# Optimization experiments

Measured on AMD Instinct MI355X. Metric: run time of the kernel, lower is better.

## Reference

```python
import jax, jax.numpy as jnp
import numpy as np
import math

D_MODEL = 1024
NUM_HEADS = 16
SEQ = 2048
BATCH = 2


def setup_inputs() -> dict:
    key = jax.random.key(0)
    ks = jax.random.split(key, 12)
    s = 1.0 / math.sqrt(D_MODEL)
    inp = {
        "query": jax.random.normal(ks[0], (SEQ, BATCH, D_MODEL), jnp.float32),
        "key": jax.random.normal(ks[1], (SEQ, BATCH, D_MODEL), jnp.float32),
        "value": jax.random.normal(ks[2], (SEQ, BATCH, D_MODEL), jnp.float32),
        "Wq": jax.random.normal(ks[3], (D_MODEL, D_MODEL), jnp.float32) * s,
        "bq": jax.random.normal(ks[4], (D_MODEL,), jnp.float32) * 0.01,
        "Wk": jax.random.normal(ks[5], (D_MODEL, D_MODEL), jnp.float32) * s,
        "bk": jax.random.normal(ks[6], (D_MODEL,), jnp.float32) * 0.01,
        "Wv": jax.random.normal(ks[7], (D_MODEL, D_MODEL), jnp.float32) * s,
        "bv": jax.random.normal(ks[8], (D_MODEL,), jnp.float32) * 0.01,
        "Wo": jax.random.normal(ks[9], (D_MODEL, D_MODEL), jnp.float32) * s,
        "bo": jax.random.normal(ks[10], (D_MODEL,), jnp.float32) * 0.01,
    }
    # causal (subsequent) mask: True above the diagonal means masked
    inp["attn_mask"] = jnp.triu(jnp.ones((SEQ, SEQ), bool), k=1)
    # key_padding_mask: True = padding; random lengths in [SEQ//2, SEQ]
    lengths = jax.random.randint(ks[11], (BATCH,), SEQ // 2, SEQ + 1)
    inp["key_padding_mask"] = jnp.arange(SEQ)[None, :] >= lengths[:, None]
    return inp


def reference(query, key, value, Wq, bq, Wk, bk, Wv, bv, Wo, bo, attn_mask, key_padding_mask):
    S, B, D = query.shape
    H = NUM_HEADS
    dk = D // H

    def proj_split(x, W, b):
        y = x @ W.T + b                      # [S, B, D]
        return y.reshape(S, B, H, dk).transpose(1, 2, 0, 3)  # [B, H, S, dk]

    q = proj_split(query, Wq, bq)
    k = proj_split(key, Wk, bk)
    v = proj_split(value, Wv, bv)

    scores = jnp.einsum("bhqd,bhkd->bhqk", q, k) / jnp.sqrt(jnp.float32(dk))
    mask = key_padding_mask[:, None, None, :] | attn_mask[None, None, :, :]
    scores = jnp.where(mask, -jnp.inf, scores)
    p = jax.nn.softmax(scores, axis=-1)       # [B, H, S, S]
    x = jnp.einsum("bhqk,bhkd->bhqd", p, v)   # [B, H, S, dk]
    x = x.transpose(2, 0, 1, 3).reshape(S, B, D)
    return x @ Wo.T + bo
```

## Files before the change

### kernel.cpp

```cpp
#include <hip/hip_runtime.h>
#include <hip/hip_bf16.h>

#define S_LEN 2048
#define BATCH 2
#define DMODEL 1024
#define NHEAD 16
#define DK 64

typedef __bf16 bf16_t;
typedef bf16_t bf16x4 __attribute__((ext_vector_type(4)));
typedef bf16_t bf16x8 __attribute__((ext_vector_type(8)));
typedef float floatx4 __attribute__((ext_vector_type(4)));

#define SEG  ((size_t)S_LEN * BATCH * DMODEL)
#define WSEG ((size_t)DMODEL * DMODEL)
#define CVT_TOT (3 * SEG + 4 * WSEG)
#define CVT_BLOCKS 4096

#define QSCALE 0.180336879f

__global__ void cvt_all(const float* __restrict__ q, const float* __restrict__ k,
                        const float* __restrict__ v, const float* __restrict__ wq,
                        const float* __restrict__ wk, const float* __restrict__ wv,
                        const float* __restrict__ wo, bf16_t* __restrict__ out,
                        const unsigned char* __restrict__ am,
                        const unsigned char* __restrict__ kpm,
                        int* __restrict__ lens)
{
    if (blockIdx.x >= CVT_BLOCKS) {
        const int b = (int)blockIdx.x - CVT_BLOCKS;
        __shared__ int cnt;
        const int t = threadIdx.x;
        if (t == 0) cnt = 0;
        int st;
        if (am[1]) st = 1;
        else if (am[2] | am[3]) st = 2;
        else st = 4;
        __syncthreads();
        int local = 0;
        for (int idx = t; idx < S_LEN; idx += blockDim.x) {
            int nz = 0;
            for (int c = 0; c < st; c++) nz |= kpm[(b * S_LEN + idx) * st + c];
            local += (nz != 0);
        }
        local += __shfl_xor(local, 1);  local += __shfl_xor(local, 2);
        local += __shfl_xor(local, 4);  local += __shfl_xor(local, 8);
        local += __shfl_xor(local, 16); local += __shfl_xor(local, 32);
        if ((t & 63) == 0) atomicAdd(&cnt, local);
        __syncthreads();
        if (t == 0) lens[b] = S_LEN - cnt;
        return;
    }

    size_t i4 = ((size_t)blockIdx.x * blockDim.x + threadIdx.x) * 4;
    const size_t stride = (size_t)CVT_BLOCKS * blockDim.x * 4;
    for (; i4 < CVT_TOT; i4 += stride) {
        const float* src;
        size_t off;
        if (i4 < SEG)                    { src = q;  off = i4; }
        else if (i4 < 2 * SEG)           { src = k;  off = i4 - SEG; }
        else if (i4 < 3 * SEG)           { src = v;  off = i4 - 2 * SEG; }
        else if (i4 < 3 * SEG + WSEG)    { src = wq; off = i4 - 3 * SEG; }
        else if (i4 < 3 * SEG + 2 * WSEG){ src = wk; off = i4 - (3 * SEG + WSEG); }
        else if (i4 < 3 * SEG + 3 * WSEG){ src = wv; off = i4 - (3 * SEG + 2 * WSEG); }
        else                             { src = wo; off = i4 - (3 * SEG + 3 * WSEG); }
        const float4 x = *(const float4*)(src + off);
        bf16x4 r;
        r[0] = (bf16_t)x.x; r[1] = (bf16_t)x.y; r[2] = (bf16_t)x.z; r[3] = (bf16_t)x.w;
        *(bf16x4*)(out + i4) = r;
    }
}

__global__ __launch_bounds__(256, 3)
void gemm_qkv(const bf16_t* __restrict__ Abase, const bf16_t* __restrict__ Wbase,
              const float* __restrict__ bq, const float* __restrict__ bk,
              const float* __restrict__ bv, bf16_t* __restrict__ Obase)
{
    __shared__ bf16_t As[2][128 * 32];
    __shared__ bf16_t Bs[2][128 * 32];

    const int L   = (int)(blockIdx.x + (blockIdx.y << 3) + (blockIdx.z << 8));
    const int xcd = L & 7;
    const int w   = L >> 3;
    const int z   = w >> 5;
    const int mBase = ((xcd << 2) | (w & 3)) * 128;
    const int nBase = ((w >> 2) & 7) * 128;

    const bf16_t* A = Abase + (size_t)z * SEG;
    const bf16_t* W = Wbase + (size_t)z * WSEG;
    const float* bias = (z == 0) ? bq : (z == 1) ? bk : bv;
    bf16_t* C = Obase + (size_t)z * SEG;

    const int t    = threadIdx.x;
    const int wave = t >> 6;
    const int lane = t & 63;
    const int l15  = lane & 15;
    const int quad = lane >> 4;

    const int wRow  = (wave >> 1) * 64;
    const int wCol  = (wave & 1) * 64;
    const int psw   = (l15 >> 1) & 3;

    floatx4 acc[4][4];
#pragma unroll
    for (int i = 0; i < 4; i++)
#pragma unroll
        for (int j = 0; j < 4; j++) acc[i][j] = (floatx4){0.f, 0.f, 0.f, 0.f};

    auto stage = [&](int k0, int buf) {
#pragma unroll
        for (int c = 0; c < 2; c++) {
            const int chunk = c * 256 + t;
            const int row   = chunk >> 2;
            const int lc    = ((chunk & 3) ^ ((row >> 1) & 3)) * 8;
            const bf16_t* gA = A + (size_t)(mBase + row) * DMODEL + k0 + lc;
            const bf16_t* gB = W + (size_t)(nBase + row) * DMODEL + k0 + lc;
            bf16_t* lA = As[buf] + (c * 256 + wave * 64) * 8;
            bf16_t* lB = Bs[buf] + (c * 256 + wave * 64) * 8;
            __builtin_amdgcn_global_load_lds(
                (const __attribute__((address_space(1))) void*)gA,
                (__attribute__((address_space(3))) void*)lA, 16, 0, 0);
            __builtin_amdgcn_global_load_lds(
                (const __attribute__((address_space(1))) void*)gB,
                (__attribute__((address_space(3))) void*)lB, 16, 0, 0);
        }
    };

    stage(0, 0);
    __syncthreads();

    for (int ks = 0; ks < DMODEL / 32; ks++) {
        const int cur = ks & 1;
        if (ks < DMODEL / 32 - 1) stage((ks + 1) * 32, cur ^ 1);

        bf16x8 af[4], bfr[4];
#pragma unroll
        for (int mi = 0; mi < 4; mi++)
            af[mi] = *(const bf16x8*)(As[cur] + (wRow + mi * 16 + l15) * 32
                                             + ((quad ^ psw)) * 8);
#pragma unroll
        for (int ni = 0; ni < 4; ni++)
            bfr[ni] = *(const bf16x8*)(Bs[cur] + (wCol + ni * 16 + l15) * 32
                                              + ((quad ^ psw)) * 8);
#pragma unroll
        for (int mi = 0; mi < 4; mi++)
#pragma unroll
            for (int ni = 0; ni < 4; ni++)
                acc[mi][ni] = __builtin_amdgcn_mfma_f32_16x16x32_bf16(
                    af[mi], bfr[ni], acc[mi][ni], 0, 0, 0);
        __syncthreads();
    }

    const float scale = (z == 0) ? QSCALE : 1.0f;
    float bvv[4];
#pragma unroll
    for (int ni = 0; ni < 4; ni++)
        bvv[ni] = bias[nBase + wCol + ni * 16 + l15];

#pragma unroll
    for (int mi = 0; mi < 4; mi++) {
#pragma unroll
        for (int ni = 0; ni < 4; ni++) {
            const int n = nBase + wCol + ni * 16 + l15;
            const int h = n >> 6, i = n & 63;
#pragma unroll
            for (int j = 0; j < 4; j++) {
                const int m = mBase + wRow + mi * 16 + quad * 4 + j;
                const int s = m >> 1, b = m & 1;
                const float v = (acc[mi][ni][j] + bvv[ni]) * scale;
                size_t off;
                if (z < 2)
                    off = ((size_t)(b * NHEAD + h) * S_LEN + s) * DK + i;
                else
                    off = ((size_t)(b * NHEAD + h) * DK + i) * S_LEN + s;
                C[off] = (bf16_t)v;
            }
        }
    }
}

__global__ __launch_bounds__(256, 4)
void attn(const bf16_t* __restrict__ qw, const bf16_t* __restrict__ kw,
          const bf16_t* __restrict__ vw, bf16_t* __restrict__ ow,
          const int* __restrict__ lens)
{
    __shared__ bf16_t Ks[2][64 * 64];
    __shared__ bf16_t Vs[2][64 * 64];
    __shared__ bf16_t Ps[4][16 * 64];

    const int t    = threadIdx.x;
    const int wave = t >> 6;
    const int lane = t & 63;
    const int l15  = lane & 15;
    const int quad = lane >> 4;
    const int qg   = lane & 48;
    const int rowbase = qg >> 2;

    const int n  = (int)(blockIdx.x + (blockIdx.y << 5));
    const int r  = n >> 8;
    const int j  = (n >> 3) & 31;
    const int bh = (n & 7) | (r << 3);
    const int flip  = (r == 1) | (r == 2);
    const int qTile = flip ? (31 - j) : j;
    const int b     = bh >> 4;
    const int len   = lens[b];
    const int qBase = qTile * 64;

    const bf16_t* kbase = kw + (size_t)bh * S_LEN * DK;
    const bf16_t* vbase = vw + (size_t)bh * DK * S_LEN;

    const int dr = lane >> 3;
    const int cc = (lane & 7) ^ dr;

    const bf16_t* Qg = qw + ((size_t)bh * S_LEN + qBase + wave * 16) * DK;
    const bf16x8 qa0 = *(const bf16x8*)(Qg + l15 * DK + quad * 8);
    const bf16x8 qa1 = *(const bf16x8*)(Qg + l15 * DK + 32 + quad * 8);

    floatx4 O[4];
#pragma unroll
    for (int i = 0; i < 4; i++) O[i] = (floatx4){0.f, 0.f, 0.f, 0.f};
    float lrow = 0.f;

    const int ktEnd = min(qTile, (len - 1) >> 6);

    auto dma_tile = [&](int ktB, int buf) {
#pragma unroll
        for (int i = 0; i < 2; i++) {
            const int R0 = (wave * 2 + i) * 8;
            const bf16_t* gK = kbase + (size_t)(ktB + R0 + dr) * DK + cc * 8;
            const bf16_t* gV = vbase + (size_t)(R0 + dr) * S_LEN + ktB + cc * 8;
            bf16_t* lK = &Ks[buf][(size_t)R0 * 64];
            bf16_t* lV = &Vs[buf][(size_t)R0 * 64];
            __builtin_amdgcn_global_load_lds(
                (const __attribute__((address_space(1))) void*)gK,
                (__attribute__((address_space(3))) void*)lK, 16, 0, 0);
            __builtin_amdgcn_global_load_lds(
                (const __attribute__((address_space(1))) void*)gV,
                (__attribute__((address_space(3))) void*)lV, 16, 0, 0);
        }
    };

    dma_tile(0, 0);
    __syncthreads();

    const int sw  = l15 & 7;
    const int ch0 = (quad ^ sw) * 8;
    const int ch1 = ((4 | quad) ^ sw) * 8;

    for (int kt = 0; kt <= ktEnd; kt++) {
        const int cur = kt & 1;
        if (kt < ktEnd) dma_tile((kt + 1) * 64, cur ^ 1);

        floatx4 sc[4];
#pragma unroll
        for (int ni = 0; ni < 4; ni++) {
            const bf16_t* kr = &Ks[cur][(ni * 16 + l15) * 64];
            const bf16x8 kf0 = *(const bf16x8*)(kr + ch0);
            const bf16x8 kf1 = *(const bf16x8*)(kr + ch1);
            floatx4 zz = (floatx4){0.f, 0.f, 0.f, 0.f};
            zz = __builtin_amdgcn_mfma_f32_16x16x32_bf16(kf0, qa0, zz, 0, 0, 0);
            zz = __builtin_amdgcn_mfma_f32_16x16x32_bf16(kf1, qa1, zz, 0, 0, 0);
            sc[ni] = zz;
        }

        const int ktBase = kt * 64;
        const int q = qBase + wave * 16 + l15;
        const bool needMask = (kt == qTile) || (ktBase + 64 > len);
        if (needMask) {
#pragma unroll
            for (int ni = 0; ni < 4; ni++) {
#pragma unroll
                for (int rr = 0; rr < 4; rr++) {
                    const int key = ktBase + ni * 16 + quad * 4 + rr;
                    if (key > q || key >= len) sc[ni][rr] = -3.0e38f;
                }
            }
        }

        float lsum = 0.f;
#pragma unroll
        for (int ni = 0; ni < 4; ni++) {
#pragma unroll
            for (int rr = 0; rr < 4; rr++) {
                const float p = exp2f(sc[ni][rr]);
                sc[ni][rr] = p;
                lsum += p;
            }
        }
        lrow += lsum;

        bf16_t* Pw = Ps[wave];
#pragma unroll
        for (int ni = 0; ni < 4; ni++) {
            bf16x4 pk;
            pk[0] = (bf16_t)sc[ni][0]; pk[1] = (bf16_t)sc[ni][1];
            pk[2] = (bf16_t)sc[ni][2]; pk[3] = (bf16_t)sc[ni][3];
            const int lc = 2 * ni + (quad >> 1);
            *(bf16x4*)(Pw + l15 * 64 + ((lc ^ sw) << 3) + (quad & 1) * 4) = pk;
        }

        const bf16x8 pa0 = *(const bf16x8*)(Pw + l15 * 64 + ((quad ^ sw) << 3));
        const bf16x8 pa1 = *(const bf16x8*)(Pw + l15 * 64 + (((4 | quad) ^ sw) << 3));
#pragma unroll
        for (int nd = 0; nd < 4; nd++) {
            const bf16_t* vr = &Vs[cur][(nd * 16 + l15) * 64];
            const bf16x8 vb0 = *(const bf16x8*)(vr + ch0);
            const bf16x8 vb1 = *(const bf16x8*)(vr + ch1);
            O[nd] = __builtin_amdgcn_mfma_f32_16x16x32_bf16(pa0, vb0, O[nd], 0, 0, 0);
            O[nd] = __builtin_amdgcn_mfma_f32_16x16x32_bf16(pa1, vb1, O[nd], 0, 0, 0);
        }
        __syncthreads();
    }

    lrow += __shfl_xor(lrow, 16);
    lrow += __shfl_xor(lrow, 32);

    float rinv[4];
#pragma unroll
    for (int jj = 0; jj < 4; jj++)
        rinv[jj] = 1.0f / __shfl(lrow, qg | (rowbase + jj));
#pragma unroll
    for (int nd = 0; nd < 4; nd++) {
        const int d = (bh & 15) * DK + nd * 16 + l15;
#pragma unroll
        for (int jj = 0; jj < 4; jj++) {
            const int qq = qBase + wave * 16 + quad * 4 + jj;
            ow[((size_t)qq * BATCH + b) * DMODEL + d] = (bf16_t)(O[nd][jj] * rinv[jj]);
        }
    }
}

__global__ __launch_bounds__(256, 2)
void gemm_o(const bf16_t* __restrict__ A, const bf16_t* __restrict__ W,
            const float* __restrict__ bias, float* __restrict__ C)
{
    __shared__ bf16_t As[2][128 * 32];
    __shared__ bf16_t Bs[2][64 * 32];

    const int L   = (int)(blockIdx.x + (blockIdx.y << 4));
    const int xcd = L & 7;
    const int w   = L >> 3;
    const int mBase = ((xcd << 2) | (w & 3)) * 128;
    const int nBase = (w >> 2) * 64;

    const int t    = threadIdx.x;
    const int wave = t >> 6;
    const int lane = t & 63;
    const int l15  = lane & 15;
    const int quad = lane >> 4;

    const int wRow  = wave * 32;
    const int psw   = (l15 >> 1) & 3;

    floatx4 acc[2][4];
#pragma unroll
    for (int i = 0; i < 2; i++)
#pragma unroll
        for (int j = 0; j < 4; j++) acc[i][j] = (floatx4){0.f, 0.f, 0.f, 0.f};

    auto stage = [&](int k0, int buf) {
#pragma unroll
        for (int c = 0; c < 2; c++) {
            const int chunk = c * 256 + t;
            const int row   = chunk >> 2;
            const int lc    = ((chunk & 3) ^ ((row >> 1) & 3)) * 8;
            const bf16_t* gA = A + (size_t)(mBase + row) * DMODEL + k0 + lc;
            bf16_t* lA = As[buf] + (c * 256 + wave * 64) * 8;
            __builtin_amdgcn_global_load_lds(
                (const __attribute__((address_space(1))) void*)gA,
                (__attribute__((address_space(3))) void*)lA, 16, 0, 0);
        }
        {
            const int row = t >> 2;
            const int lc  = ((t & 3) ^ ((row >> 1) & 3)) * 8;
            const bf16_t* gB = W + (size_t)(nBase + row) * DMODEL + k0 + lc;
            bf16_t* lB = Bs[buf] + (wave * 64) * 8;
            __builtin_amdgcn_global_load_lds(
                (const __attribute__((address_space(1))) void*)gB,
                (__attribute__((address_space(3))) void*)lB, 16, 0, 0);
        }
    };

    stage(0, 0);
    __syncthreads();

    for (int ks = 0; ks < DMODEL / 32; ks++) {
        const int cur = ks & 1;
        if (ks < DMODEL / 32 - 1) stage((ks + 1) * 32, cur ^ 1);

        bf16x8 af[2], bfr[4];
#pragma unroll
        for (int mi = 0; mi < 2; mi++)
            af[mi] = *(const bf16x8*)(As[cur] + (wRow + mi * 16 + l15) * 32
                                             + ((quad ^ psw)) * 8);
#pragma unroll
        for (int ni = 0; ni < 4; ni++)
            bfr[ni] = *(const bf16x8*)(Bs[cur] + (ni * 16 + l15) * 32
                                              + ((quad ^ psw)) * 8);
#pragma unroll
        for (int mi = 0; mi < 2; mi++)
#pragma unroll
            for (int ni = 0; ni < 4; ni++)
                acc[mi][ni] = __builtin_amdgcn_mfma_f32_16x16x32_bf16(
                    af[mi], bfr[ni], acc[mi][ni], 0, 0, 0);
        __syncthreads();
    }

    float bvv[4];
#pragma unroll
    for (int ni = 0; ni < 4; ni++)
        bvv[ni] = bias[nBase + ni * 16 + l15];

#pragma unroll
    for (int mi = 0; mi < 2; mi++) {
#pragma unroll
        for (int ni = 0; ni < 4; ni++) {
            const int n = nBase + ni * 16 + l15;
#pragma unroll
            for (int j = 0; j < 4; j++) {
                const int m = mBase + wRow + mi * 16 + quad * 4 + j;
                C[(size_t)m * DMODEL + n] = acc[mi][ni][j] + bvv[ni];
            }
        }
    }
}

extern "C" void kernel_launch(void* const* d_in, const int* in_sizes, int n_in,
                              void* d_out, int out_size, void* d_ws, size_t ws_size,
                              hipStream_t stream)
{
    const float* query = (const float*)d_in[0];
    const float* key   = (const float*)d_in[1];
    const float* value = (const float*)d_in[2];
    const float* Wq = (const float*)d_in[3];
    const float* bq = (const float*)d_in[4];
    const float* Wk = (const float*)d_in[5];
    const float* bk = (const float*)d_in[6];
    const float* Wv = (const float*)d_in[7];
    const float* bv = (const float*)d_in[8];
    const float* Wo = (const float*)d_in[9];
    const float* bo = (const float*)d_in[10];
    const unsigned char* am  = (const unsigned char*)d_in[11];
    const unsigned char* kpm = (const unsigned char*)d_in[12];

    bf16_t* cvt   = (bf16_t*)d_ws;
    bf16_t* q_bf  = cvt;
    bf16_t* wq_bf = cvt + 3 * SEG;
    bf16_t* wo_bf = wq_bf + 3 * WSEG;
    bf16_t* q_ws  = cvt + CVT_TOT;
    bf16_t* k_ws  = q_ws + SEG;
    bf16_t* v_ws  = k_ws + SEG;
    bf16_t* o_ws  = q_bf;
    int*    lens  = (int*)(v_ws + SEG);

    cvt_all<<<CVT_BLOCKS + BATCH, 256, 0, stream>>>(
        query, key, value, Wq, Wk, Wv, Wo, cvt, am, kpm, lens);

    gemm_qkv<<<dim3(DMODEL / 128, (S_LEN * BATCH) / 128, 3), dim3(256), 0, stream>>>(
        q_bf, wq_bf, bq, bk, bv, q_ws);

    attn<<<dim3(32, BATCH * NHEAD), dim3(256), 0, stream>>>(
        q_ws, k_ws, v_ws, o_ws, lens);

    gemm_o<<<dim3(DMODEL / 64, (S_LEN * BATCH) / 128), dim3(256), 0, stream>>>(
        o_ws, wo_bf, bo, (float*)d_out);
}
```

Measured before the change: 236.4 us.

## Fuse fp32-to-bf16 conversion into GEMM staging and drop the conversion kernel

```diff
diff --git a/kernel.cpp b/kernel.cpp
--- a/kernel.cpp
+++ b/kernel.cpp
@@ -13,22 +13,30 @@
 typedef float floatx4 __attribute__((ext_vector_type(4)));
 
 #define SEG  ((size_t)S_LEN * BATCH * DMODEL)
-#define WSEG ((size_t)DMODEL * DMODEL)
-#define CVT_TOT (3 * SEG + 4 * WSEG)
-#define CVT_BLOCKS 4096
 
 #define QSCALE 0.180336879f
 
-__global__ void cvt_all(const float* __restrict__ q, const float* __restrict__ k,
-                        const float* __restrict__ v, const float* __restrict__ wq,
-                        const float* __restrict__ wk, const float* __restrict__ wv,
-                        const float* __restrict__ wo, bf16_t* __restrict__ out,
-                        const unsigned char* __restrict__ am,
-                        const unsigned char* __restrict__ kpm,
-                        int* __restrict__ lens)
+__device__ __forceinline__ bf16x8 pack8(float4 x, float4 y)
 {
-    if (blockIdx.x >= CVT_BLOCKS) {
-        const int b = (int)blockIdx.x - CVT_BLOCKS;
+    bf16x8 r;
+    r[0] = (bf16_t)x.x; r[1] = (bf16_t)x.y; r[2] = (bf16_t)x.z; r[3] = (bf16_t)x.w;
+    r[4] = (bf16_t)y.x; r[5] = (bf16_t)y.y; r[6] = (bf16_t)y.z; r[7] = (bf16_t)y.w;
+    return r;
+}
+
+__global__ __launch_bounds__(256, 3)
+void gemm_qkv(const float* __restrict__ qf, const float* __restrict__ kf,
+              const float* __restrict__ vf, const float* __restrict__ wqf,
+              const float* __restrict__ wkf, const float* __restrict__ wvf,
+              const float* __restrict__ bq, const float* __restrict__ bk,
+              const float* __restrict__ bv, bf16_t* __restrict__ Obase,
+              const unsigned char* __restrict__ am,
+              const unsigned char* __restrict__ kpm,
+              int* __restrict__ lens)
+{
+    const int L = (int)blockIdx.x;
+    if (L >= 768) {
+        const int b = L - 768;
         __shared__ int cnt;
         const int t = threadIdx.x;
         if (t == 0) cnt = 0;
@@ -38,7 +46,7 @@
         else st = 4;
         __syncthreads();
         int local = 0;
-        for (int idx = t; idx < S_LEN; idx += blockDim.x) {
+        for (int idx = t; idx < S_LEN; idx += 256) {
             int nz = 0;
             for (int c = 0; c < st; c++) nz |= kpm[(b * S_LEN + idx) * st + c];
             local += (nz != 0);
@@ -52,43 +60,18 @@
         return;
     }
 
-    size_t i4 = ((size_t)blockIdx.x * blockDim.x + threadIdx.x) * 4;
-    const size_t stride = (size_t)CVT_BLOCKS * blockDim.x * 4;
-    for (; i4 < CVT_TOT; i4 += stride) {
-        const float* src;
-        size_t off;
-        if (i4 < SEG)                    { src = q;  off = i4; }
-        else if (i4 < 2 * SEG)           { src = k;  off = i4 - SEG; }
-        else if (i4 < 3 * SEG)           { src = v;  off = i4 - 2 * SEG; }
-        else if (i4 < 3 * SEG + WSEG)    { src = wq; off = i4 - 3 * SEG; }
-        else if (i4 < 3 * SEG + 2 * WSEG){ src = wk; off = i4 - (3 * SEG + WSEG); }
-        else if (i4 < 3 * SEG + 3 * WSEG){ src = wv; off = i4 - (3 * SEG + 2 * WSEG); }
-        else                             { src = wo; off = i4 - (3 * SEG + 3 * WSEG); }
-        const float4 x = *(const float4*)(src + off);
-        bf16x4 r;
-        r[0] = (bf16_t)x.x; r[1] = (bf16_t)x.y; r[2] = (bf16_t)x.z; r[3] = (bf16_t)x.w;
-        *(bf16x4*)(out + i4) = r;
-    }
-}
-
-__global__ __launch_bounds__(256, 3)
-void gemm_qkv(const bf16_t* __restrict__ Abase, const bf16_t* __restrict__ Wbase,
-              const float* __restrict__ bq, const float* __restrict__ bk,
-              const float* __restrict__ bv, bf16_t* __restrict__ Obase)
-{
     __shared__ bf16_t As[2][128 * 32];
     __shared__ bf16_t Bs[2][128 * 32];
 
-    const int L   = (int)(blockIdx.x + (blockIdx.y << 3) + (blockIdx.z << 8));
     const int xcd = L & 7;
     const int w   = L >> 3;
     const int z   = w >> 5;
     const int mBase = ((xcd << 2) | (w & 3)) * 128;
     const int nBase = ((w >> 2) & 7) * 128;
 
-    const bf16_t* A = Abase + (size_t)z * SEG;
-    const bf16_t* W = Wbase + (size_t)z * WSEG;
-    const float* bias = (z == 0) ? bq : (z == 1) ? bk : bv;
+    const float* A    = (z == 0) ? qf  : (z == 1) ? kf  : vf;
+    const float* W    = (z == 0) ? wqf : (z == 1) ? wkf : wvf;
+    const float* bias = (z == 0) ? bq  : (z == 1) ? bk  : bv;
     bf16_t* C = Obase + (size_t)z * SEG;
 
     const int t    = threadIdx.x;
@@ -101,53 +84,61 @@
     const int wCol  = (wave & 1) * 64;
     const int psw   = (l15 >> 1) & 3;
 
+    const int row0 = t >> 2;
+    const int row1 = 64 + row0;
+    const int col8 = (t & 3) * 8;
+    const int pc0  = (((t & 3) ^ ((row0 >> 1) & 3))) * 8;
+    const int pc1  = (((t & 3) ^ ((row1 >> 1) & 3))) * 8;
+
+    float4 ra[2][2], rb[2][2];
+    auto stage_load = [&](int k0) {
+        const float* gA0 = A + (size_t)(mBase + row0) * DMODEL + k0 + col8;
+        const float* gA1 = A + (size_t)(mBase + row1) * DMODEL + k0 + col8;
+        const float* gB0 = W + (size_t)(nBase + row0) * DMODEL + k0 + col8;
+        const float* gB1 = W + (size_t)(nBase + row1) * DMODEL + k0 + col8;
+        ra[0][0] = ((const float4*)gA0)[0]; ra[0][1] = ((const float4*)gA0)[1];
+        ra[1][0] = ((const float4*)gA1)[0]; ra[1][1] = ((const float4*)gA1)[1];
+        rb[0][0] = ((const float4*)gB0)[0]; rb[0][1] = ((const float4*)gB0)[1];
+        rb[1][0] = ((const float4*)gB1)[0]; rb[1][1] = ((const float4*)gB1)[1];
+    };
+    auto stage_write = [&](int buf) {
+        *(bf16x8*)(As[buf] + row0 * 32 + pc0) = pack8(ra[0][0], ra[0][1]);
+        *(bf16x8*)(As[buf] + row1 * 32 + pc1) = pack8(ra[1][0], ra[1][1]);
+        *(bf16x8*)(Bs[buf] + row0 * 32 + pc0) = pack8(rb[0][0], rb[0][1]);
+        *(bf16x8*)(Bs[buf] + row1 * 32 + pc1) = pack8(rb[1][0], rb[1][1]);
+    };
+
     floatx4 acc[4][4];
 #pragma unroll
     for (int i = 0; i < 4; i++)
 #pragma unroll
         for (int j = 0; j < 4; j++) acc[i][j] = (floatx4){0.f, 0.f, 0.f, 0.f};
 
-    auto stage = [&](int k0, int buf) {
-#pragma unroll
-        for (int c = 0; c < 2; c++) {
-            const int chunk = c * 256 + t;
-            const int row   = chunk >> 2;
-            const int lc    = ((chunk & 3) ^ ((row >> 1) & 3)) * 8;
-            const bf16_t* gA = A + (size_t)(mBase + row) * DMODEL + k0 + lc;
-            const bf16_t* gB = W + (size_t)(nBase + row) * DMODEL + k0 + lc;
-            bf16_t* lA = As[buf] + (c * 256 + wave * 64) * 8;
-            bf16_t* lB = Bs[buf] + (c * 256 + wave * 64) * 8;
-            __builtin_amdgcn_global_load_lds(
-                (const __attribute__((address_space(1))) void*)gA,
-                (__attribute__((address_space(3))) void*)lA, 16, 0, 0);
-            __builtin_amdgcn_global_load_lds(
-                (const __attribute__((address_space(1))) void*)gB,
-                (__attribute__((address_space(3))) void*)lB, 16, 0, 0);
-        }
-    };
-
-    stage(0, 0);
+    stage_load(0);
+    stage_write(0);
     __syncthreads();
 
     for (int ks = 0; ks < DMODEL / 32; ks++) {
         const int cur = ks & 1;
-        if (ks < DMODEL / 32 - 1) stage((ks + 1) * 32, cur ^ 1);
+        if (ks < DMODEL / 32 - 1) stage_load((ks + 1) * 32);
 
         bf16x8 af[4], bfr[4];
 #pragma unroll
         for (int mi = 0; mi < 4; mi++)
             af[mi] = *(const bf16x8*)(As[cur] + (wRow + mi * 16 + l15) * 32
-                                             + ((quad ^ psw)) * 8);
+                                             + (quad ^ psw) * 8);
 #pragma unroll
         for (int ni = 0; ni < 4; ni++)
             bfr[ni] = *(const bf16x8*)(Bs[cur] + (wCol + ni * 16 + l15) * 32
-                                              + ((quad ^ psw)) * 8);
+                                              + (quad ^ psw) * 8);
 #pragma unroll
         for (int mi = 0; mi < 4; mi++)
 #pragma unroll
             for (int ni = 0; ni < 4; ni++)
                 acc[mi][ni] = __builtin_amdgcn_mfma_f32_16x16x32_bf16(
                     af[mi], bfr[ni], acc[mi][ni], 0, 0, 0);
+
+        if (ks < DMODEL / 32 - 1) stage_write(cur ^ 1);
         __syncthreads();
     }
 
@@ -331,13 +322,13 @@
 }
 
 __global__ __launch_bounds__(256, 2)
-void gemm_o(const bf16_t* __restrict__ A, const bf16_t* __restrict__ W,
+void gemm_o(const bf16_t* __restrict__ A, const float* __restrict__ W,
             const float* __restrict__ bias, float* __restrict__ C)
 {
     __shared__ bf16_t As[2][128 * 32];
     __shared__ bf16_t Bs[2][64 * 32];
 
-    const int L   = (int)(blockIdx.x + (blockIdx.y << 4));
+    const int L   = (int)blockIdx.x;
     const int xcd = L & 7;
     const int w   = L >> 3;
     const int mBase = ((xcd << 2) | (w & 3)) * 128;
@@ -352,13 +343,20 @@
     const int wRow  = wave * 32;
     const int psw   = (l15 >> 1) & 3;
 
-    floatx4 acc[2][4];
-#pragma unroll
-    for (int i = 0; i < 2; i++)
-#pragma unroll
-        for (int j = 0; j < 4; j++) acc[i][j] = (floatx4){0.f, 0.f, 0.f, 0.f};
-
-    auto stage = [&](int k0, int buf) {
+    const int brow = t >> 2;
+    const int bcol = (t & 3) * 8;
+    const int bpc  = (((t & 3) ^ ((brow >> 1) & 3))) * 8;
+
+    float4 rb[2];
+    auto b_load = [&](int k0) {
+        const float* gB = W + (size_t)(nBase + brow) * DMODEL + k0 + bcol;
+        rb[0] = ((const float4*)gB)[0];
+        rb[1] = ((const float4*)gB)[1];
+    };
+    auto b_write = [&](int buf) {
+        *(bf16x8*)(Bs[buf] + brow * 32 + bpc) = pack8(rb[0], rb[1]);
+    };
+    auto stageA = [&](int k0, int buf) {
 #pragma unroll
         for (int c = 0; c < 2; c++) {
             const int chunk = c * 256 + t;
@@ -370,39 +368,43 @@
                 (const __attribute__((address_space(1))) void*)gA,
                 (__attribute__((address_space(3))) void*)lA, 16, 0, 0);
         }
-        {
-            const int row = t >> 2;
-            const int lc  = ((t & 3) ^ ((row >> 1) & 3)) * 8;
-            const bf16_t* gB = W + (size_t)(nBase + row) * DMODEL + k0 + lc;
-            bf16_t* lB = Bs[buf] + (wave * 64) * 8;
-            __builtin_amdgcn_global_load_lds(
-                (const __attribute__((address_space(1))) void*)gB,
-                (__attribute__((address_space(3))) void*)lB, 16, 0, 0);
-        }
-    };
-
-    stage(0, 0);
+    };
+
+    floatx4 acc[2][4];
+#pragma unroll
+    for (int i = 0; i < 2; i++)
+#pragma unroll
+        for (int j = 0; j < 4; j++) acc[i][j] = (floatx4){0.f, 0.f, 0.f, 0.f};
+
+    stageA(0, 0);
+    b_load(0);
+    b_write(0);
     __syncthreads();
 
     for (int ks = 0; ks < DMODEL / 32; ks++) {
         const int cur = ks & 1;
-        if (ks < DMODEL / 32 - 1) stage((ks + 1) * 32, cur ^ 1);
+        if (ks < DMODEL / 32 - 1) {
+            stageA((ks + 1) * 32, cur ^ 1);
+            b_load((ks + 1) * 32);
+        }
 
         bf16x8 af[2], bfr[4];
 #pragma unroll
         for (int mi = 0; mi < 2; mi++)
             af[mi] = *(const bf16x8*)(As[cur] + (wRow + mi * 16 + l15) * 32
-                                             + ((quad ^ psw)) * 8);
+                                             + (quad ^ psw) * 8);
 #pragma unroll
         for (int ni = 0; ni < 4; ni++)
             bfr[ni] = *(const bf16x8*)(Bs[cur] + (ni * 16 + l15) * 32
-                                              + ((quad ^ psw)) * 8);
+                                              + (quad ^ psw) * 8);
 #pragma unroll
         for (int mi = 0; mi < 2; mi++)
 #pragma unroll
             for (int ni = 0; ni < 4; ni++)
                 acc[mi][ni] = __builtin_amdgcn_mfma_f32_16x16x32_bf16(
                     af[mi], bfr[ni], acc[mi][ni], 0, 0, 0);
+
+        if (ks < DMODEL / 32 - 1) b_write(cur ^ 1);
         __syncthreads();
     }
 
@@ -443,25 +445,18 @@
     const unsigned char* am  = (const unsigned char*)d_in[11];
     const unsigned char* kpm = (const unsigned char*)d_in[12];
 
-    bf16_t* cvt   = (bf16_t*)d_ws;
-    bf16_t* q_bf  = cvt;
-    bf16_t* wq_bf = cvt + 3 * SEG;
-    bf16_t* wo_bf = wq_bf + 3 * WSEG;
-    bf16_t* q_ws  = cvt + CVT_TOT;
-    bf16_t* k_ws  = q_ws + SEG;
-    bf16_t* v_ws  = k_ws + SEG;
-    bf16_t* o_ws  = q_bf;
-    int*    lens  = (int*)(v_ws + SEG);
-
-    cvt_all<<<CVT_BLOCKS + BATCH, 256, 0, stream>>>(
-        query, key, value, Wq, Wk, Wv, Wo, cvt, am, kpm, lens);
-
-    gemm_qkv<<<dim3(DMODEL / 128, (S_LEN * BATCH) / 128, 3), dim3(256), 0, stream>>>(
-        q_bf, wq_bf, bq, bk, bv, q_ws);
+    bf16_t* q_ws = (bf16_t*)d_ws;
+    bf16_t* k_ws = q_ws + SEG;
+    bf16_t* v_ws = k_ws + SEG;
+    bf16_t* o_ws = v_ws + SEG;
+    int*    lens = (int*)(o_ws + SEG);
+
+    gemm_qkv<<<770, 256, 0, stream>>>(
+        query, key, value, Wq, Wk, Wv, bq, bk, bv, q_ws, am, kpm, lens);
 
     attn<<<dim3(32, BATCH * NHEAD), dim3(256), 0, stream>>>(
         q_ws, k_ws, v_ws, o_ws, lens);
 
-    gemm_o<<<dim3(DMODEL / 64, (S_LEN * BATCH) / 128), dim3(256), 0, stream>>>(
-        o_ws, wo_bf, bo, (float*)d_out);
+    gemm_o<<<512, 256, 0, stream>>>(
+        o_ws, Wo, bo, (float*)d_out);
 }
```

Result: slower. 273.0 us (+15.5%).

## Fuse fp32-to-bf16 activation conversion into QKV GEMM A-tile loads

Applied to the files above, without the earlier changes.

```diff
diff --git a/kernel.cpp b/kernel.cpp
--- a/kernel.cpp
+++ b/kernel.cpp
@@ -14,21 +14,28 @@
 
 #define SEG  ((size_t)S_LEN * BATCH * DMODEL)
 #define WSEG ((size_t)DMODEL * DMODEL)
-#define CVT_TOT (3 * SEG + 4 * WSEG)
-#define CVT_BLOCKS 4096
 
 #define QSCALE 0.180336879f
 
-__global__ void cvt_all(const float* __restrict__ q, const float* __restrict__ k,
-                        const float* __restrict__ v, const float* __restrict__ wq,
-                        const float* __restrict__ wk, const float* __restrict__ wv,
-                        const float* __restrict__ wo, bf16_t* __restrict__ out,
-                        const unsigned char* __restrict__ am,
-                        const unsigned char* __restrict__ kpm,
-                        int* __restrict__ lens)
-{
-    if (blockIdx.x >= CVT_BLOCKS) {
-        const int b = (int)blockIdx.x - CVT_BLOCKS;
+__device__ __forceinline__ bf16x8 pack8(float4 x, float4 y)
+{
+    bf16x8 r;
+    r[0] = (bf16_t)x.x; r[1] = (bf16_t)x.y; r[2] = (bf16_t)x.z; r[3] = (bf16_t)x.w;
+    r[4] = (bf16_t)y.x; r[5] = (bf16_t)y.y; r[6] = (bf16_t)y.z; r[7] = (bf16_t)y.w;
+    return r;
+}
+
+#define CVTW_BLOCKS 2048
+#define CVTW_TOT (4 * WSEG)
+__global__ void cvt_w(const float* __restrict__ wq, const float* __restrict__ wk,
+                      const float* __restrict__ wv, const float* __restrict__ wo,
+                      bf16_t* __restrict__ out,
+                      const unsigned char* __restrict__ am,
+                      const unsigned char* __restrict__ kpm,
+                      int* __restrict__ lens)
+{
+    if (blockIdx.x >= CVTW_BLOCKS) {
+        const int b = (int)blockIdx.x - CVTW_BLOCKS;
         __shared__ int cnt;
         const int t = threadIdx.x;
         if (t == 0) cnt = 0;
@@ -38,7 +45,7 @@
         else st = 4;
         __syncthreads();
         int local = 0;
-        for (int idx = t; idx < S_LEN; idx += blockDim.x) {
+        for (int idx = t; idx < S_LEN; idx += 256) {
             int nz = 0;
             for (int c = 0; c < st; c++) nz |= kpm[(b * S_LEN + idx) * st + c];
             local += (nz != 0);
@@ -53,17 +60,14 @@
     }
 
     size_t i4 = ((size_t)blockIdx.x * blockDim.x + threadIdx.x) * 4;
-    const size_t stride = (size_t)CVT_BLOCKS * blockDim.x * 4;
-    for (; i4 < CVT_TOT; i4 += stride) {
+    const size_t stride = (size_t)CVTW_BLOCKS * blockDim.x * 4;
+    for (; i4 < CVTW_TOT; i4 += stride) {
         const float* src;
         size_t off;
-        if (i4 < SEG)                    { src = q;  off = i4; }
-        else if (i4 < 2 * SEG)           { src = k;  off = i4 - SEG; }
-        else if (i4 < 3 * SEG)           { src = v;  off = i4 - 2 * SEG; }
-        else if (i4 < 3 * SEG + WSEG)    { src = wq; off = i4 - 3 * SEG; }
-        else if (i4 < 3 * SEG + 2 * WSEG){ src = wk; off = i4 - (3 * SEG + WSEG); }
-        else if (i4 < 3 * SEG + 3 * WSEG){ src = wv; off = i4 - (3 * SEG + 2 * WSEG); }
-        else                             { src = wo; off = i4 - (3 * SEG + 3 * WSEG); }
+        if (i4 < WSEG)          { src = wq; off = i4; }
+        else if (i4 < 2 * WSEG) { src = wk; off = i4 - WSEG; }
+        else if (i4 < 3 * WSEG) { src = wv; off = i4 - 2 * WSEG; }
+        else                    { src = wo; off = i4 - 3 * WSEG; }
         const float4 x = *(const float4*)(src + off);
         bf16x4 r;
         r[0] = (bf16_t)x.x; r[1] = (bf16_t)x.y; r[2] = (bf16_t)x.z; r[3] = (bf16_t)x.w;
@@ -72,23 +76,24 @@
 }
 
 __global__ __launch_bounds__(256, 3)
-void gemm_qkv(const bf16_t* __restrict__ Abase, const bf16_t* __restrict__ Wbase,
+void gemm_qkv(const float* __restrict__ qf, const float* __restrict__ kf,
+              const float* __restrict__ vf, const bf16_t* __restrict__ Wbase,
               const float* __restrict__ bq, const float* __restrict__ bk,
               const float* __restrict__ bv, bf16_t* __restrict__ Obase)
 {
-    __shared__ bf16_t As[2][128 * 32];
+    __shared__ float  Af[2][128 * 32];
     __shared__ bf16_t Bs[2][128 * 32];
 
-    const int L   = (int)(blockIdx.x + (blockIdx.y << 3) + (blockIdx.z << 8));
+    const int L   = (int)blockIdx.x;
     const int xcd = L & 7;
     const int w   = L >> 3;
     const int z   = w >> 5;
     const int mBase = ((xcd << 2) | (w & 3)) * 128;
     const int nBase = ((w >> 2) & 7) * 128;
 
-    const bf16_t* A = Abase + (size_t)z * SEG;
-    const bf16_t* W = Wbase + (size_t)z * WSEG;
-    const float* bias = (z == 0) ? bq : (z == 1) ? bk : bv;
+    const float*  A    = (z == 0) ? qf : (z == 1) ? kf : vf;
+    const bf16_t* W    = Wbase + (size_t)z * WSEG;
+    const float*  bias = (z == 0) ? bq : (z == 1) ? bk : bv;
     bf16_t* C = Obase + (size_t)z * SEG;
 
     const int t    = threadIdx.x;
@@ -100,6 +105,10 @@
     const int wRow  = (wave >> 1) * 64;
     const int wCol  = (wave & 1) * 64;
     const int psw   = (l15 >> 1) & 3;
+    const int swa   = l15 & 7;
+
+    const int dr = lane >> 3;
+    const int cc = (lane & 7) ^ dr;
 
     floatx4 acc[4][4];
 #pragma unroll
@@ -108,18 +117,22 @@
         for (int j = 0; j < 4; j++) acc[i][j] = (floatx4){0.f, 0.f, 0.f, 0.f};
 
     auto stage = [&](int k0, int buf) {
+#pragma unroll
+        for (int i = 0; i < 4; i++) {
+            const int R0 = (wave * 4 + i) * 8;
+            const float* gA = A + (size_t)(mBase + R0 + dr) * DMODEL + k0 + cc * 4;
+            float* lA = &Af[buf][(size_t)R0 * 32];
+            __builtin_amdgcn_global_load_lds(
+                (const __attribute__((address_space(1))) void*)gA,
+                (__attribute__((address_space(3))) void*)lA, 16, 0, 0);
+        }
 #pragma unroll
         for (int c = 0; c < 2; c++) {
             const int chunk = c * 256 + t;
             const int row   = chunk >> 2;
             const int lc    = ((chunk & 3) ^ ((row >> 1) & 3)) * 8;
-            const bf16_t* gA = A + (size_t)(mBase + row) * DMODEL + k0 + lc;
             const bf16_t* gB = W + (size_t)(nBase + row) * DMODEL + k0 + lc;
-            bf16_t* lA = As[buf] + (c * 256 + wave * 64) * 8;
             bf16_t* lB = Bs[buf] + (c * 256 + wave * 64) * 8;
-            __builtin_amdgcn_global_load_lds(
-                (const __attribute__((address_space(1))) void*)gA,
-                (__attribute__((address_space(3))) void*)lA, 16, 0, 0);
             __builtin_amdgcn_global_load_lds(
                 (const __attribute__((address_space(1))) void*)gB,
                 (__attribute__((address_space(3))) void*)lB, 16, 0, 0);
@@ -135,13 +148,16 @@
 
         bf16x8 af[4], bfr[4];
 #pragma unroll
-        for (int mi = 0; mi < 4; mi++)
-            af[mi] = *(const bf16x8*)(As[cur] + (wRow + mi * 16 + l15) * 32
-                                             + ((quad ^ psw)) * 8);
+        for (int mi = 0; mi < 4; mi++) {
+            const float* ar = &Af[cur][(size_t)(wRow + mi * 16 + l15) * 32];
+            const float4 lo = *(const float4*)(ar + ((2 * quad) ^ swa) * 4);
+            const float4 hi = *(const float4*)(ar + ((2 * quad + 1) ^ swa) * 4);
+            af[mi] = pack8(lo, hi);
+        }
 #pragma unroll
         for (int ni = 0; ni < 4; ni++)
             bfr[ni] = *(const bf16x8*)(Bs[cur] + (wCol + ni * 16 + l15) * 32
-                                              + ((quad ^ psw)) * 8);
+                                              + (quad ^ psw) * 8);
 #pragma unroll
         for (int mi = 0; mi < 4; mi++)
 #pragma unroll
@@ -337,7 +353,7 @@
     __shared__ bf16_t As[2][128 * 32];
     __shared__ bf16_t Bs[2][64 * 32];
 
-    const int L   = (int)(blockIdx.x + (blockIdx.y << 4));
+    const int L   = (int)blockIdx.x;
     const int xcd = L & 7;
     const int w   = L >> 3;
     const int mBase = ((xcd << 2) | (w & 3)) * 128;
@@ -351,12 +367,6 @@
 
     const int wRow  = wave * 32;
     const int psw   = (l15 >> 1) & 3;
-
-    floatx4 acc[2][4];
-#pragma unroll
-    for (int i = 0; i < 2; i++)
-#pragma unroll
-        for (int j = 0; j < 4; j++) acc[i][j] = (floatx4){0.f, 0.f, 0.f, 0.f};
 
     auto stage = [&](int k0, int buf) {
 #pragma unroll
@@ -381,6 +391,12 @@
         }
     };
 
+    floatx4 acc[2][4];
+#pragma unroll
+    for (int i = 0; i < 2; i++)
+#pragma unroll
+        for (int j = 0; j < 4; j++) acc[i][j] = (floatx4){0.f, 0.f, 0.f, 0.f};
+
     stage(0, 0);
     __syncthreads();
 
@@ -392,11 +408,11 @@
 #pragma unroll
         for (int mi = 0; mi < 2; mi++)
             af[mi] = *(const bf16x8*)(As[cur] + (wRow + mi * 16 + l15) * 32
-                                             + ((quad ^ psw)) * 8);
+                                             + (quad ^ psw) * 8);
 #pragma unroll
         for (int ni = 0; ni < 4; ni++)
             bfr[ni] = *(const bf16x8*)(Bs[cur] + (ni * 16 + l15) * 32
-                                              + ((quad ^ psw)) * 8);
+                                              + (quad ^ psw) * 8);
 #pragma unroll
         for (int mi = 0; mi < 2; mi++)
 #pragma unroll
@@ -443,25 +459,23 @@
     const unsigned char* am  = (const unsigned char*)d_in[11];
     const unsigned char* kpm = (const unsigned char*)d_in[12];
 
-    bf16_t* cvt   = (bf16_t*)d_ws;
-    bf16_t* q_bf  = cvt;
-    bf16_t* wq_bf = cvt + 3 * SEG;
-    bf16_t* wo_bf = wq_bf + 3 * WSEG;
-    bf16_t* q_ws  = cvt + CVT_TOT;
+    bf16_t* w_bf  = (bf16_t*)d_ws;
+    bf16_t* wo_bf = w_bf + 3 * WSEG;
+    bf16_t* q_ws  = w_bf + 4 * WSEG;
     bf16_t* k_ws  = q_ws + SEG;
     bf16_t* v_ws  = k_ws + SEG;
-    bf16_t* o_ws  = q_bf;
-    int*    lens  = (int*)(v_ws + SEG);
-
-    cvt_all<<<CVT_BLOCKS + BATCH, 256, 0, stream>>>(
-        query, key, value, Wq, Wk, Wv, Wo, cvt, am, kpm, lens);
-
-    gemm_qkv<<<dim3(DMODEL / 128, (S_LEN * BATCH) / 128, 3), dim3(256), 0, stream>>>(
-        q_bf, wq_bf, bq, bk, bv, q_ws);
+    bf16_t* o_ws  = v_ws + SEG;
+    int*    lens  = (int*)(o_ws + SEG);
+
+    cvt_w<<<CVTW_BLOCKS + BATCH, 256, 0, stream>>>(
+        Wq, Wk, Wv, Wo, w_bf, am, kpm, lens);
+
+    gemm_qkv<<<768, 256, 0, stream>>>(
+        query, key, value, w_bf, bq, bk, bv, q_ws);
 
     attn<<<dim3(32, BATCH * NHEAD), dim3(256), 0, stream>>>(
         q_ws, k_ws, v_ws, o_ws, lens);
 
-    gemm_o<<<dim3(DMODEL / 64, (S_LEN * BATCH) / 128), dim3(256), 0, stream>>>(
+    gemm_o<<<512, 256, 0, stream>>>(
         o_ws, wo_bf, bo, (float*)d_out);
 }
```

After: 252.9 us. +7.0%, slower.
